# Optimization experiments

Measured on AMD Instinct MI355X. Metric: run time of the kernel, lower is better.

## Reference

```python
import jax, jax.numpy as jnp
import numpy as np

B, C, D, H, W = 4, 256, 16, 16, 16
REDUCTION = 8
CR = C // REDUCTION  # q/k channel dim = 32


def setup_inputs() -> dict:
    key = jax.random.key(0)
    k1, k2, k3, k4, k5, k6 = jax.random.split(key, 6)
    x = jax.random.normal(k1, (B, C, D, H, W), dtype=jnp.float32)
    # 1x1x1 conv weights are just [out_ch, in_ch] matrices
    Wq = jax.random.normal(k2, (CR, C), dtype=jnp.float32) * (1.0 / np.sqrt(C))
    Wk = jax.random.normal(k3, (CR, C), dtype=jnp.float32) * (1.0 / np.sqrt(C))
    Wv = jax.random.normal(k4, (C, C), dtype=jnp.float32) * (1.0 / np.sqrt(C))
    Wo = jax.random.normal(k5, (C, C), dtype=jnp.float32) * (1.0 / np.sqrt(C))
    gamma = jnp.zeros((1,), dtype=jnp.float32) + 0.5  # nonzero so output depends on attention
    return {"x": x, "Wq": Wq, "Wk": Wk, "Wv": Wv, "Wo": Wo, "gamma": gamma}


def reference(x, Wq, Wk, Wv, Wo, gamma):
    b, c, d, h, w = x.shape
    n = d * h * w
    scale = Wq.shape[0] ** -0.5  # (channels // reduction) ** -0.5
    xf = x.reshape(b, c, n)                      # [B, C, N]
    q = jnp.einsum('oc,bcn->bon', Wq, xf)        # [B, CR, N]
    k = jnp.einsum('oc,bcn->bon', Wk, xf)        # [B, CR, N]
    v = jnp.einsum('oc,bcn->bon', Wv, xf)        # [B, C, N]
    attn = jax.nn.softmax(jnp.einsum('bcn,bcm->bnm', q, k) * scale, axis=-1)  # [B, N, N]
    out = jnp.einsum('bcm,bnm->bcn', v, attn)    # v @ attn^T -> [B, C, N]
    out = jnp.einsum('oc,bcn->bon', Wo, out)     # output 1x1x1 conv
    out = out.reshape(b, c, d, h, w)
    return gamma[0] * out + x
```

## Files before the change

kernel.cpp:

```cpp
#include <hip/hip_runtime.h>
#include <hip/hip_bf16.h>

#define BATCH 4
#define CH 256
#define CRD 32
#define NN 4096

typedef __bf16 bf16x8 __attribute__((ext_vector_type(8)));
typedef float floatx4 __attribute__((ext_vector_type(4)));
typedef float floatx16 __attribute__((ext_vector_type(16)));
typedef unsigned short ushort4v __attribute__((ext_vector_type(4)));
typedef unsigned short ushort8v __attribute__((ext_vector_type(8)));

static __device__ __forceinline__ unsigned short f2bf(float f) {
    unsigned int u = __float_as_uint(f);
    u += 0x7fff + ((u >> 16) & 1);
    return (unsigned short)(u >> 16);
}
static __device__ __forceinline__ float bf2f(unsigned short h) {
    return __uint_as_float((unsigned int)h << 16);
}


__global__ __launch_bounds__(256) void wconv_kernel(
    const float* __restrict__ Wq, const float* __restrict__ Wk,
    const float* __restrict__ Wv, const float* __restrict__ Wo,
    unsigned short* __restrict__ What, unsigned short* __restrict__ WobF)
{
    const int o = blockIdx.x;
    const int t = threadIdx.x;
    float scale = 1.0f;
    const float* src;
    if (o < 32)      { src = Wq + o * 256; scale = 0.17677669529663687f; }
    else if (o < 64) { src = Wk + (o - 32) * 256; }
    else             { src = Wv + (o - 64) * 256; }
    const int mb = o >> 5;
    const size_t idx = ((size_t)(mb * 16 + (t >> 4)) * 64
                        + (o & 31) + 32 * ((t >> 3) & 1)) * 8 + (t & 7);
    What[idx] = f2bf(src[t] * scale);
    if (o < 256) {
        const size_t i2 = ((size_t)((o >> 5) * 16 + (t >> 4)) * 64
                           + (o & 31) + 32 * ((t >> 3) & 1)) * 8 + (t & 7);
        WobF[i2] = f2bf(Wo[o * 256 + t]);
    }
}

__global__ __launch_bounds__(256, 2) void qkv_kernel(
    const float* __restrict__ x, const unsigned short* __restrict__ What,
    unsigned short* __restrict__ qh, unsigned short* __restrict__ kh,
    unsigned short* __restrict__ vh)
{
    __shared__ unsigned short xf[16 * 512];

    const int t = threadIdx.x;
    const int w = t >> 6;
    const int l = t & 63;
    const int l31 = l & 31;
    const int h = l >> 5;
    const int nt = blockIdx.x, b = blockIdx.y;
    const int n0 = nt * 32;

    {
        const float* xb = x + (size_t)(b * CH) * NN + n0;
        const int n = t & 31;
        const int cq = t >> 5;
        #pragma unroll
        for (int p = 0; p < 8; ++p) {
            int c = p * 32 + cq * 4;
            float v0 = xb[(size_t)(c + 0) * NN + n];
            float v1 = xb[(size_t)(c + 1) * NN + n];
            float v2 = xb[(size_t)(c + 2) * NN + n];
            float v3 = xb[(size_t)(c + 3) * NN + n];
            ushort4v u4;
            u4[0] = f2bf(v0); u4[1] = f2bf(v1); u4[2] = f2bf(v2); u4[3] = f2bf(v3);
            int addr = ((2 * p + (cq >> 2)) * 64 + n + 32 * ((cq >> 1) & 1)) * 8
                       + 4 * (cq & 1);
            *(ushort4v*)&xf[addr] = u4;
        }
    }
    __syncthreads();

    const int mb0 = w, mb1 = w + 4, mb2 = w + 8;
    floatx16 acc0, acc1, acc2;
    #pragma unroll
    for (int i = 0; i < 16; ++i) { acc0[i] = 0.f; acc1[i] = 0.f; acc2[i] = 0.f; }

    for (int kblk = 0; kblk < 16; ++kblk) {
        bf16x8 bf = *(const bf16x8*)&xf[kblk * 512 + l * 8];
        bf16x8 a0 = *(const bf16x8*)(What + ((size_t)(mb0 * 16 + kblk) * 64 + l) * 8);
        bf16x8 a1 = *(const bf16x8*)(What + ((size_t)(mb1 * 16 + kblk) * 64 + l) * 8);
        acc0 = __builtin_amdgcn_mfma_f32_32x32x16_bf16(a0, bf, acc0, 0, 0, 0);
        acc1 = __builtin_amdgcn_mfma_f32_32x32x16_bf16(a1, bf, acc1, 0, 0, 0);
        if (w < 2) {
            bf16x8 a2 = *(const bf16x8*)(What + ((size_t)(mb2 * 16 + kblk) * 64 + l) * 8);
            acc2 = __builtin_amdgcn_mfma_f32_32x32x16_bf16(a2, bf, acc2, 0, 0, 0);
        }
    }

    auto store_qk = [&](unsigned short* dst, const floatx16& a) {
        size_t base = (size_t)(b * 128 + nt) * 1024;
        #pragma unroll
        for (int rg = 0; rg < 4; ++rg) {
            ushort4v u4;
            #pragma unroll
            for (int i = 0; i < 4; ++i) u4[i] = f2bf(a[rg * 4 + i]);
            size_t idx = base + (size_t)(rg >> 1) * 512
                         + (size_t)(l31 + 32 * (rg & 1)) * 8 + 4 * h;
            *(ushort4v*)(dst + idx) = u4;
        }
    };
    auto store_v = [&](int cblk, const floatx16& a) {
        size_t base = (((size_t)b * 8 + cblk) * 256 + nt * 2 + (l31 >> 4)) * 512
                      + 32 * ((l31 >> 3) & 1) * 8 + (l31 & 7);
        #pragma unroll
        for (int r = 0; r < 16; ++r) {
            int rowo = (r & 3) + 8 * (r >> 2) + 4 * h;
            vh[base + rowo * 8] = f2bf(a[r]);
        }
    };

    if (w == 0)      store_qk(qh, acc0);
    else if (w == 1) store_qk(kh, acc0);
    else             store_v(w - 2, acc0);
    store_v(w + 2, acc1);
    if (w < 2) store_v(w + 6, acc2);
}

__global__ __launch_bounds__(256, 4) void attn_kernel(
    const unsigned short* __restrict__ qh, const unsigned short* __restrict__ kh,
    const unsigned short* __restrict__ vh, unsigned short* __restrict__ Opart,
    float* __restrict__ ml)
{
    __shared__ unsigned short p_lds[8 * 64 * 8];
    __shared__ float pmax_s[4][32];
    __shared__ float psum_s[4][32];

    const int t = threadIdx.x;
    const int w = t >> 6;
    const int l = t & 63;
    const int l31 = l & 31;
    const int h = l >> 5;
    const int g = blockIdx.x, ks = blockIdx.y, b = blockIdx.z;

    const unsigned short* qB = qh + (size_t)(b * 128 + g) * 1024;
    const unsigned short* kB = kh + (size_t)b * 128 * 1024;
    const unsigned short* vB = vh + (size_t)b * 8 * 256 * 512;

    bf16x8 qf0 = *(const bf16x8*)(qB + l * 8);
    bf16x8 qf1 = *(const bf16x8*)(qB + 512 + l * 8);

    bf16x8 kf0 = *(const bf16x8*)(kB + (size_t)(ks * 32 + w) * 1024 + l * 8);
    bf16x8 kf1 = *(const bf16x8*)(kB + (size_t)(ks * 32 + w) * 1024 + 512 + l * 8);

    float m_run = -1e30f, l_run = 0.f;
    floatx16 acc0, acc1;
    #pragma unroll
    for (int i = 0; i < 16; ++i) { acc0[i] = 0.f; acc1[i] = 0.f; }

    for (int it = 0; it < 8; ++it) {
        floatx16 sacc;
        #pragma unroll
        for (int i = 0; i < 16; ++i) sacc[i] = 0.f;
        sacc = __builtin_amdgcn_mfma_f32_32x32x16_bf16(kf0, qf0, sacc, 0, 0, 0);
        sacc = __builtin_amdgcn_mfma_f32_32x32x16_bf16(kf1, qf1, sacc, 0, 0, 0);

        float pm = sacc[0];
        #pragma unroll
        for (int r = 1; r < 16; ++r) pm = fmaxf(pm, sacc[r]);
        pm = fmaxf(pm, __shfl_xor(pm, 32));
        if (h == 0) pmax_s[w][l31] = pm;
        __syncthreads();

        float mnew = fmaxf(fmaxf(pmax_s[0][l31], pmax_s[1][l31]),
                           fmaxf(pmax_s[2][l31], pmax_s[3][l31]));
        mnew = fmaxf(m_run, mnew);
        float alpha = __expf(m_run - mnew);
        m_run = mnew;
        float pv[16];
        float psum = 0.f;
        #pragma unroll
        for (int r = 0; r < 16; ++r) {
            pv[r] = __expf(sacc[r] - mnew);
            psum += pv[r];
        }
        psum += __shfl_xor(psum, 32);
        if (h == 0) psum_s[w][l31] = psum;
        #pragma unroll
        for (int rg = 0; rg < 4; ++rg) {
            ushort4v pk;
            #pragma unroll
            for (int i = 0; i < 4; ++i) pk[i] = f2bf(pv[rg * 4 + i]);
            int idx = ((2 * w + (rg >> 1)) * 64 + l31 + 32 * (rg & 1)) * 8 + 4 * h;
            *(ushort4v*)&p_lds[idx] = pk;
        }
        if (it < 7) {
            const unsigned short* kn = kB + (size_t)(ks * 32 + (it + 1) * 4 + w) * 1024;
            kf0 = *(const bf16x8*)(kn + l * 8);
            kf1 = *(const bf16x8*)(kn + 512 + l * 8);
        }
        __syncthreads();

        float isum = (psum_s[0][l31] + psum_s[1][l31]) +
                     (psum_s[2][l31] + psum_s[3][l31]);
        l_run = l_run * alpha + isum;
        #pragma unroll
        for (int i = 0; i < 16; ++i) { acc0[i] *= alpha; acc1[i] *= alpha; }

        const unsigned short* v0b = vB + ((size_t)(2 * w) * 256 + (ks * 8 + it) * 8) * 512;
        const unsigned short* v1b = vB + ((size_t)(2 * w + 1) * 256 + (ks * 8 + it) * 8) * 512;
        bf16x8 va = *(const bf16x8*)(v0b + l * 8);
        bf16x8 vc = *(const bf16x8*)(v1b + l * 8);
        bf16x8 pf = *(const bf16x8*)&p_lds[l * 8];
        #pragma unroll
        for (int s = 0; s < 8; ++s) {
            bf16x8 va_n, vc_n, pf_n;
            if (s < 7) {
                va_n = *(const bf16x8*)(v0b + (s + 1) * 512 + l * 8);
                vc_n = *(const bf16x8*)(v1b + (s + 1) * 512 + l * 8);
                pf_n = *(const bf16x8*)&p_lds[((s + 1) * 64 + l) * 8];
            }
            acc0 = __builtin_amdgcn_mfma_f32_32x32x16_bf16(va, pf, acc0, 0, 0, 0);
            acc1 = __builtin_amdgcn_mfma_f32_32x32x16_bf16(vc, pf, acc1, 0, 0, 0);
            va = va_n; vc = vc_n; pf = pf_n;
        }
    }

    unsigned short* op = Opart + ((size_t)((b * 128 + g) * 4 + ks)) * 8192;
    #pragma unroll
    for (int ct = 0; ct < 2; ++ct) {
        const floatx16& a = ct ? acc1 : acc0;
        #pragma unroll
        for (int rg = 0; rg < 4; ++rg) {
            ushort4v pk;
            #pragma unroll
            for (int i = 0; i < 4; ++i) pk[i] = f2bf(a[rg * 4 + i]);
            int sP = 4 * w + 2 * ct + (rg >> 1);
            size_t idx = ((size_t)sP * 64 + l31 + 32 * (rg & 1)) * 8 + 4 * h;
            *(ushort4v*)(op + idx) = pk;
        }
    }
    if (w == 0 && h == 0) {
        size_t mb = ((size_t)(b * 128 + g) * 4 + ks) * 64;
        ml[mb + l31] = m_run;
        ml[mb + 32 + l31] = l_run;
    }
}

__global__ __launch_bounds__(256, 2) void out_kernel(
    const unsigned short* __restrict__ Opart, const float* __restrict__ ml,
    const unsigned short* __restrict__ WobF, const float* __restrict__ x,
    const float* __restrict__ gamma, float* __restrict__ out)
{
    const int t = threadIdx.x;
    const int w = t >> 6;
    const int l = t & 63;
    const int l31 = l & 31;
    const int h = l >> 5;
    const int qt = blockIdx.x, b = blockIdx.y;

    const size_t slot = (size_t)(b * 128 + qt) * 4;
    float m0 = ml[(slot + 0) * 64 + l31], l0 = ml[(slot + 0) * 64 + 32 + l31];
    float m1 = ml[(slot + 1) * 64 + l31], l1 = ml[(slot + 1) * 64 + 32 + l31];
    float m2 = ml[(slot + 2) * 64 + l31], l2 = ml[(slot + 2) * 64 + 32 + l31];
    float m3 = ml[(slot + 3) * 64 + l31], l3 = ml[(slot + 3) * 64 + 32 + l31];
    float M = fmaxf(fmaxf(m0, m1), fmaxf(m2, m3));
    float e0 = __expf(m0 - M), e1 = __expf(m1 - M);
    float e2 = __expf(m2 - M), e3 = __expf(m3 - M);
    float Lc = l0 * e0 + l1 * e1 + l2 * e2 + l3 * e3;
    float w0 = e0 / Lc, w1 = e1 / Lc, w2 = e2 / Lc, w3 = e3 / Lc;

    const unsigned short* o0 = Opart + (slot + 0) * 8192;
    const unsigned short* o1 = Opart + (slot + 1) * 8192;
    const unsigned short* o2 = Opart + (slot + 2) * 8192;
    const unsigned short* o3 = Opart + (slot + 3) * 8192;

    floatx16 acc[2];
    #pragma unroll
    for (int m = 0; m < 2; ++m)
        #pragma unroll
        for (int i = 0; i < 16; ++i) acc[m][i] = 0.f;

    for (int s = 0; s < 16; ++s) {
        ushort8v f0 = *(const ushort8v*)(o0 + (s * 64 + l) * 8);
        ushort8v f1 = *(const ushort8v*)(o1 + (s * 64 + l) * 8);
        ushort8v f2 = *(const ushort8v*)(o2 + (s * 64 + l) * 8);
        ushort8v f3 = *(const ushort8v*)(o3 + (s * 64 + l) * 8);
        ushort8v cmb;
        #pragma unroll
        for (int j = 0; j < 8; ++j)
            cmb[j] = f2bf(w0 * bf2f(f0[j]) + w1 * bf2f(f1[j])
                        + w2 * bf2f(f2[j]) + w3 * bf2f(f3[j]));
        bf16x8 bfr = *(bf16x8*)&cmb;
        #pragma unroll
        for (int m = 0; m < 2; ++m) {
            int mt = 2 * w + m;
            bf16x8 af = *(const bf16x8*)(WobF + ((size_t)(mt * 16 + s) * 64 + l) * 8);
            acc[m] = __builtin_amdgcn_mfma_f32_32x32x16_bf16(af, bfr, acc[m], 0, 0, 0);
        }
    }

    const float gm = gamma[0];
    #pragma unroll
    for (int m = 0; m < 2; ++m)
        #pragma unroll
        for (int r = 0; r < 16; ++r) {
            int o = (2 * w + m) * 32 + (r & 3) + 8 * (r >> 2) + 4 * h;
            int n = qt * 32 + l31;
            size_t oi = ((size_t)(b * 256 + o)) * NN + n;
            out[oi] = gm * acc[m][r] + x[oi];
        }
}

extern "C" void kernel_launch(void* const* d_in, const int* in_sizes, int n_in,
                              void* d_out, int out_size, void* d_ws, size_t ws_size,
                              hipStream_t stream)
{
    const float* x     = (const float*)d_in[0];
    const float* Wq    = (const float*)d_in[1];
    const float* Wk    = (const float*)d_in[2];
    const float* Wv    = (const float*)d_in[3];
    const float* Wo    = (const float*)d_in[4];
    const float* gamma = (const float*)d_in[5];
    float* out = (float*)d_out;

    char* wsb = (char*)d_ws;
    unsigned short* qh    = (unsigned short*)(wsb);
    unsigned short* kh    = (unsigned short*)(wsb + (1u << 20));
    unsigned short* vh    = (unsigned short*)(wsb + (2u << 20));
    unsigned short* What  = (unsigned short*)(wsb + (10u << 20));
    unsigned short* WobF  = (unsigned short*)(wsb + (10u << 20) + (256u << 10));
    unsigned short* Opart = (unsigned short*)(wsb + (11u << 20));
    float*          ml    = (float*)         (wsb + (45u << 20));

    wconv_kernel<<<320, 256, 0, stream>>>(Wq, Wk, Wv, Wo, What, WobF);

    dim3 g1(128, BATCH);
    qkv_kernel<<<g1, 256, 0, stream>>>(x, What, qh, kh, vh);

    dim3 g2(128, 4, BATCH);
    attn_kernel<<<g2, 256, 0, stream>>>(qh, kh, vh, Opart, ml);

    dim3 g3(128, BATCH);
    out_kernel<<<g3, 256, 0, stream>>>(Opart, ml, WobF, x, gamma, out);
}
```

Before: 161.9 us.

## Use exp2 with folded log2e, wider merged stores, block remap, and MFMA priority

Folds log2(e) into the Q weight scale so softmax can use exp2 directly in the attention and combine kernels. Replaces the manual bf16 rounding with a hardware conversion, and merges the half-wave ushort4 stores into 16-byte stores through lane shuffles. It also remaps the attention grid's block index so blocks sharing the same batch's K/V run close together, raises wave priority around the MFMAs, uses tree reductions for max and sum, and computes one reciprocal instead of four divisions. The extra shuffles cost a few instructions, and the conversion intrinsic may handle NaN differently from the manual rounding.

```diff
diff --git a/kernel.cpp b/kernel.cpp
--- a/kernel.cpp
+++ b/kernel.cpp
@@ -11,11 +11,12 @@
 typedef float floatx16 __attribute__((ext_vector_type(16)));
 typedef unsigned short ushort4v __attribute__((ext_vector_type(4)));
 typedef unsigned short ushort8v __attribute__((ext_vector_type(8)));
+typedef unsigned int uint2v __attribute__((ext_vector_type(2)));
+typedef unsigned int uint4v __attribute__((ext_vector_type(4)));
 
 static __device__ __forceinline__ unsigned short f2bf(float f) {
-    unsigned int u = __float_as_uint(f);
-    u += 0x7fff + ((u >> 16) & 1);
-    return (unsigned short)(u >> 16);
+    __bf16 h = (__bf16)f;
+    return __builtin_bit_cast(unsigned short, h);
 }
 static __device__ __forceinline__ float bf2f(unsigned short h) {
     return __uint_as_float((unsigned int)h << 16);
@@ -31,7 +32,8 @@
     const int t = threadIdx.x;
     float scale = 1.0f;
     const float* src;
-    if (o < 32)      { src = Wq + o * 256; scale = 0.17677669529663687f; }
+    if (o < 32)      { src = Wq + o * 256;
+                       scale = 0.17677669529663687f * 1.4426950408889634f; }
     else if (o < 64) { src = Wk + (o - 32) * 256; }
     else             { src = Wv + (o - 64) * 256; }
     const int mb = o >> 5;
@@ -43,6 +45,23 @@
                            + (o & 31) + 32 * ((t >> 3) & 1)) * 8 + (t & 7);
         WobF[i2] = f2bf(Wo[o * 256 + t]);
     }
+}
+
+static __device__ __forceinline__ uint4v hmerge(
+    const ushort4v& xp, const ushort4v& yp, int h)
+{
+    uint2v xd = __builtin_bit_cast(uint2v, xp);
+    uint2v yd = __builtin_bit_cast(uint2v, yp);
+    unsigned int px0 = (unsigned int)__shfl_xor((int)xd[0], 32);
+    unsigned int px1 = (unsigned int)__shfl_xor((int)xd[1], 32);
+    unsigned int py0 = (unsigned int)__shfl_xor((int)yd[0], 32);
+    unsigned int py1 = (unsigned int)__shfl_xor((int)yd[1], 32);
+    uint4v st;
+    st[0] = h ? py0 : xd[0];
+    st[1] = h ? py1 : xd[1];
+    st[2] = h ? yd[0] : px0;
+    st[3] = h ? yd[1] : px1;
+    return st;
 }
 
 __global__ __launch_bounds__(256, 2) void qkv_kernel(
@@ -100,13 +119,15 @@
     auto store_qk = [&](unsigned short* dst, const floatx16& a) {
         size_t base = (size_t)(b * 128 + nt) * 1024;
         #pragma unroll
-        for (int rg = 0; rg < 4; ++rg) {
-            ushort4v u4;
+        for (int sb = 0; sb < 2; ++sb) {
+            ushort4v xp, yp;
             #pragma unroll
-            for (int i = 0; i < 4; ++i) u4[i] = f2bf(a[rg * 4 + i]);
-            size_t idx = base + (size_t)(rg >> 1) * 512
-                         + (size_t)(l31 + 32 * (rg & 1)) * 8 + 4 * h;
-            *(ushort4v*)(dst + idx) = u4;
+            for (int i = 0; i < 4; ++i) {
+                xp[i] = f2bf(a[8 * sb + i]);
+                yp[i] = f2bf(a[8 * sb + 4 + i]);
+            }
+            uint4v st = hmerge(xp, yp, h);
+            *(uint4v*)(dst + base + (size_t)sb * 512 + (size_t)l * 8) = st;
         }
     };
     auto store_v = [&](int cblk, const floatx16& a) {
@@ -140,7 +161,13 @@
     const int l = t & 63;
     const int l31 = l & 31;
     const int h = l >> 5;
-    const int g = blockIdx.x, ks = blockIdx.y, b = blockIdx.z;
+
+    const int lin = blockIdx.x + ((int)blockIdx.y << 7) + ((int)blockIdx.z << 9);
+    const int slot = lin >> 3;
+    const int combo = ((lin & 7) << 1) | (slot >> 7);
+    const int g  = slot & 127;
+    const int ks = combo & 3;
+    const int b  = combo >> 2;
 
     const unsigned short* qB = qh + (size_t)(b * 128 + g) * 1024;
     const unsigned short* kB = kh + (size_t)b * 128 * 1024;
@@ -161,12 +188,16 @@
         floatx16 sacc;
         #pragma unroll
         for (int i = 0; i < 16; ++i) sacc[i] = 0.f;
+        __builtin_amdgcn_s_setprio(1);
         sacc = __builtin_amdgcn_mfma_f32_32x32x16_bf16(kf0, qf0, sacc, 0, 0, 0);
         sacc = __builtin_amdgcn_mfma_f32_32x32x16_bf16(kf1, qf1, sacc, 0, 0, 0);
-
-        float pm = sacc[0];
-        #pragma unroll
-        for (int r = 1; r < 16; ++r) pm = fmaxf(pm, sacc[r]);
+        __builtin_amdgcn_s_setprio(0);
+
+        float t0 = fmaxf(fmaxf(sacc[0], sacc[1]),  fmaxf(sacc[2], sacc[3]));
+        float t1 = fmaxf(fmaxf(sacc[4], sacc[5]),  fmaxf(sacc[6], sacc[7]));
+        float t2 = fmaxf(fmaxf(sacc[8], sacc[9]),  fmaxf(sacc[10], sacc[11]));
+        float t3 = fmaxf(fmaxf(sacc[12], sacc[13]), fmaxf(sacc[14], sacc[15]));
+        float pm = fmaxf(fmaxf(t0, t1), fmaxf(t2, t3));
         pm = fmaxf(pm, __shfl_xor(pm, 32));
         if (h == 0) pmax_s[w][l31] = pm;
         __syncthreads();
@@ -174,15 +205,16 @@
         float mnew = fmaxf(fmaxf(pmax_s[0][l31], pmax_s[1][l31]),
                            fmaxf(pmax_s[2][l31], pmax_s[3][l31]));
         mnew = fmaxf(m_run, mnew);
-        float alpha = __expf(m_run - mnew);
+        float alpha = __builtin_exp2f(m_run - mnew);
         m_run = mnew;
         float pv[16];
-        float psum = 0.f;
-        #pragma unroll
-        for (int r = 0; r < 16; ++r) {
-            pv[r] = __expf(sacc[r] - mnew);
-            psum += pv[r];
-        }
+        #pragma unroll
+        for (int r = 0; r < 16; ++r) pv[r] = __builtin_exp2f(sacc[r] - mnew);
+        float s0 = (pv[0] + pv[1]) + (pv[2] + pv[3]);
+        float s1 = (pv[4] + pv[5]) + (pv[6] + pv[7]);
+        float s2 = (pv[8] + pv[9]) + (pv[10] + pv[11]);
+        float s3 = (pv[12] + pv[13]) + (pv[14] + pv[15]);
+        float psum = (s0 + s1) + (s2 + s3);
         psum += __shfl_xor(psum, 32);
         if (h == 0) psum_s[w][l31] = psum;
         #pragma unroll
@@ -219,8 +251,10 @@
                 vc_n = *(const bf16x8*)(v1b + (s + 1) * 512 + l * 8);
                 pf_n = *(const bf16x8*)&p_lds[((s + 1) * 64 + l) * 8];
             }
+            __builtin_amdgcn_s_setprio(1);
             acc0 = __builtin_amdgcn_mfma_f32_32x32x16_bf16(va, pf, acc0, 0, 0, 0);
             acc1 = __builtin_amdgcn_mfma_f32_32x32x16_bf16(vc, pf, acc1, 0, 0, 0);
+            __builtin_amdgcn_s_setprio(0);
             va = va_n; vc = vc_n; pf = pf_n;
         }
     }
@@ -230,13 +264,16 @@
     for (int ct = 0; ct < 2; ++ct) {
         const floatx16& a = ct ? acc1 : acc0;
         #pragma unroll
-        for (int rg = 0; rg < 4; ++rg) {
-            ushort4v pk;
+        for (int sb = 0; sb < 2; ++sb) {
+            ushort4v xp, yp;
             #pragma unroll
-            for (int i = 0; i < 4; ++i) pk[i] = f2bf(a[rg * 4 + i]);
-            int sP = 4 * w + 2 * ct + (rg >> 1);
-            size_t idx = ((size_t)sP * 64 + l31 + 32 * (rg & 1)) * 8 + 4 * h;
-            *(ushort4v*)(op + idx) = pk;
+            for (int i = 0; i < 4; ++i) {
+                xp[i] = f2bf(a[8 * sb + i]);
+                yp[i] = f2bf(a[8 * sb + 4 + i]);
+            }
+            uint4v st = hmerge(xp, yp, h);
+            int sP = 4 * w + 2 * ct + sb;
+            *(uint4v*)(op + ((size_t)sP * 64 + l) * 8) = st;
         }
     }
     if (w == 0 && h == 0) {
@@ -264,10 +301,11 @@
     float m2 = ml[(slot + 2) * 64 + l31], l2 = ml[(slot + 2) * 64 + 32 + l31];
     float m3 = ml[(slot + 3) * 64 + l31], l3 = ml[(slot + 3) * 64 + 32 + l31];
     float M = fmaxf(fmaxf(m0, m1), fmaxf(m2, m3));
-    float e0 = __expf(m0 - M), e1 = __expf(m1 - M);
-    float e2 = __expf(m2 - M), e3 = __expf(m3 - M);
+    float e0 = __builtin_exp2f(m0 - M), e1 = __builtin_exp2f(m1 - M);
+    float e2 = __builtin_exp2f(m2 - M), e3 = __builtin_exp2f(m3 - M);
     float Lc = l0 * e0 + l1 * e1 + l2 * e2 + l3 * e3;
-    float w0 = e0 / Lc, w1 = e1 / Lc, w2 = e2 / Lc, w3 = e3 / Lc;
+    float rL = 1.0f / Lc;
+    float w0 = e0 * rL, w1 = e1 * rL, w2 = e2 * rL, w3 = e3 * rL;
 
     const unsigned short* o0 = Opart + (slot + 0) * 8192;
     const unsigned short* o1 = Opart + (slot + 1) * 8192;
```

Result: no change. 160.6 us (-0.8%).
